# Performance work log

Measured on AMD Instinct MI355X. Metric: run time of the kernel, lower is better.

## Reference

```python
import jax, jax.numpy as jnp
import numpy as np
from functools import partial

CONF_THRESH = 0.5
NMS_THRESH = 0.5
B, N, NUM_CLASSES = 2, 10647, 80


def setup_inputs() -> dict:
    key = jax.random.key(0)
    # [batch, num_bboxes, x,y,w,h,p_obj + 80 class scores], uniform in [0,1)
    x = jax.random.uniform(key, (B, N, 5 + NUM_CLASSES), dtype=jnp.float32)
    return {"x": x}


def _center_to_corner(b):
    # b: [N,4] = (cx, cy, w, h) -> (x1, y1, x2, y2)
    cx, cy, w, h = b[:, 0], b[:, 1], b[:, 2], b[:, 3]
    return jnp.stack([cx - w / 2, cy - h / 2, cx + w / 2, cy + h / 2], axis=1)


def _pairwise_iou(b):
    # b: [N,4] corner boxes -> [N,N] IoU
    x1, y1, x2, y2 = b[:, 0], b[:, 1], b[:, 2], b[:, 3]
    ix1 = jnp.maximum(x1[:, None], x1[None, :])
    iy1 = jnp.maximum(y1[:, None], y1[None, :])
    ix2 = jnp.minimum(x2[:, None], x2[None, :])
    iy2 = jnp.minimum(y2[:, None], y2[None, :])
    inter = jnp.clip(ix2 - ix1, 0.0) * jnp.clip(iy2 - iy1, 0.0)
    area = (x2 - x1) * (y2 - y1)
    union = area[:, None] + area[None, :] - inter
    return inter / jnp.maximum(union, 1e-9)


def _nms_image(x_img, batch_idx):
    # x_img: [N, 5+C]. Faithful to the torch loop: conf-filter, per-class
    # greedy IoU suppression in descending-confidence order.
    n = x_img.shape[0]
    valid = x_img[:, 4] > CONF_THRESH
    xm = x_img * valid[:, None].astype(x_img.dtype)  # zero out background rows
    boxes = _center_to_corner(xm[:, :4])
    conf = xm[:, 4]
    score = jnp.max(xm[:, 5:], axis=1)
    cls = jnp.argmax(xm[:, 5:], axis=1)

    # Sort by confidence (descending) so greedy order matches the torch sort.
    order = jnp.argsort(-conf)
    boxes_s, cls_s, valid_s = boxes[order], cls[order], valid[order]

    # Suppression matrix: same class AND IoU >= threshold (constant wrt grads).
    iou = _pairwise_iou(boxes_s)                      # [N,N]
    same = cls_s[:, None] == cls_s[None, :]
    sup_mat = jax.lax.stop_gradient((iou >= NMS_THRESH) & same)

    idxs = jnp.arange(n)

    def body(i, keep):
        # box i (if still kept) suppresses lower-confidence same-class overlaps
        sup = keep[i] & (idxs > i) & sup_mat[i]
        return keep & ~sup

    keep_s = jax.lax.fori_loop(0, n, body, valid_s)
    keep = jnp.zeros(n, bool).at[order].set(keep_s)   # unsort

    km = keep[:, None].astype(x_img.dtype)
    bcol = jnp.full((n, 1), batch_idx, dtype=x_img.dtype) * km
    det = jnp.concatenate(
        [bcol, boxes * km, (conf * keep)[:, None],
         (score * keep)[:, None], (cls.astype(x_img.dtype) * keep)[:, None]],
        axis=1)  # [N, 8]: batch_idx, x1,y1,x2,y2, p_obj, max_conf, cls_idx
    return det


def reference(x) -> jnp.ndarray:
    batch_ids = jnp.arange(x.shape[0], dtype=x.dtype)
    # [B, N, 8]; suppressed / background rows are all-zero (fixed-shape analogue
    # of the variable-length torch detections tensor).
    return jax.vmap(_nms_image)(x, batch_ids)
```

## Files before the change

kernel.cpp:

```cpp
#include <hip/hip_runtime.h>
#include <stdint.h>

#define NROWS 10647
#define NFEAT 85
#define NCLS  80
#define NIMG  2
#define CONF_TH 0.5f
#define IOU_TH  0.5f
#define CAP    256
#define ROWS_PB 128

__global__ void k_zero(int* __restrict__ ccnt) {
    if (threadIdx.x < NIMG * NCLS) ccnt[threadIdx.x] = 0;
}

__global__ __launch_bounds__(256) void k_compact(
    const float* __restrict__ x, float4* __restrict__ bbox,
    float4* __restrict__ bmisc, int* __restrict__ ccnt, float* __restrict__ out) {
    __shared__ float buf[ROWS_PB * NFEAT];
    int img  = blockIdx.y;
    int base = blockIdx.x * ROWS_PB;
    int nrow = min(ROWS_PB, NROWS - base);
    int nflt = nrow * NFEAT;
    const float* g = x + ((size_t)img * NROWS + base) * NFEAT;
    const float4* g4 = (const float4*)g;
    float4* b4 = (float4*)buf;
    int nv = nflt >> 2;
    for (int i = threadIdx.x; i < nv; i += 256) b4[i] = g4[i];
    for (int i = (nv << 2) + threadIdx.x; i < nflt; i += 256) buf[i] = g[i];
    if (threadIdx.x < nrow) {
        float4 z = make_float4(0.f, 0.f, 0.f, 0.f);
        float4* o = (float4*)(out + ((size_t)img * NROWS + base + threadIdx.x) * 8);
        o[0] = z; o[1] = z;
    }
    __syncthreads();
    int t = threadIdx.x;
    if (t >= nrow) return;
    const float* row = buf + t * NFEAT;
    float conf = row[4];
    if (!(conf > CONF_TH)) return;
    float cx = row[0], cy = row[1], w = row[2], h = row[3];
    float4 b = make_float4(cx - w * 0.5f, cy - h * 0.5f,
                           cx + w * 0.5f, cy + h * 0.5f);
    float best = row[5];
    int cls = 0;
    for (int c = 1; c < NCLS; ++c) {
        float v = row[5 + c];
        if (v > best) { best = v; cls = c; }
    }
    int r = base + t;
    int pos = atomicAdd(&ccnt[img * NCLS + cls], 1);
    if (pos >= CAP) return;
    int idx = (img * NCLS + cls) * CAP + pos;
    bbox[idx]  = b;
    bmisc[idx] = make_float4(conf, best, (float)cls, __int_as_float(r));
}

__global__ __launch_bounds__(64) void k_nms(
    const float4* __restrict__ bbox, const float4* __restrict__ bmisc,
    const int* __restrict__ ccnt, float* __restrict__ out) {
    int cls = blockIdx.x, img = blockIdx.y;
    int mc = min(ccnt[img * NCLS + cls], CAP);
    if (mc == 0) return;
    int lane = threadIdx.x;
    int bse  = (img * NCLS + cls) * CAP;
    __shared__ uint64_t kl[CAP];
    __shared__ float4   sb[CAP];
    __shared__ float4   sm[CAP];

    float4 rb[4], rm[4];
    #pragma unroll
    for (int q = 0; q < 4; ++q) {
        int e = (q << 6) + lane;
        if (e < mc) {
            rb[q] = bbox[bse + e];
            rm[q] = bmisc[bse + e];
            uint32_t cbits = __float_as_uint(rm[q].x);
            kl[e] = ((uint64_t)(~cbits) << 32) | (uint32_t)__float_as_int(rm[q].w);
        }
    }
    __syncthreads();
    #pragma unroll
    for (int q = 0; q < 4; ++q) {
        int e = (q << 6) + lane;
        if (e < mc) {
            uint64_t k = kl[e];
            int rank = 0;
            for (int u = 0; u < mc; ++u) rank += (kl[u] < k);
            sb[rank] = rb[q];
            sm[rank] = rm[q];
        }
    }
    __syncthreads();
    float4 cb[4], cm[4];
    #pragma unroll
    for (int q = 0; q < 4; ++q) {
        int e = (q << 6) + lane;
        if (e < mc) { cb[q] = sb[e]; cm[q] = sm[e]; }
    }
    uint64_t km[4];
    #pragma unroll
    for (int q = 0; q < 4; ++q) {
        int lo = q << 6;
        km[q] = (mc >= lo + 64) ? ~0ull : (mc > lo ? ((1ull << (mc - lo)) - 1) : 0ull);
    }

#define SUPW(QI, QJ)                                                          \
    if ((QJ) * 64 < mc) {                                                     \
        bool s_ = false;                                                      \
        int j_ = ((QJ) << 6) + lane;                                          \
        if (j_ < mc && ((QJ) > (QI) || lane > li)) {                          \
            float bx = cb[QJ].x, by = cb[QJ].y, bz = cb[QJ].z, bw = cb[QJ].w; \
            float ix1 = fmaxf(ax, bx), iy1 = fmaxf(ay, by);                   \
            float ix2 = fminf(az, bz), iy2 = fminf(aw, bw);                   \
            float inter = fmaxf(ix2 - ix1, 0.f) * fmaxf(iy2 - iy1, 0.f);      \
            float ab = (bz - bx) * (bw - by);                                 \
            float iou = inter / fmaxf((aa + ab) - inter, 1e-9f);              \
            s_ = (iou >= IOU_TH);                                             \
        }                                                                     \
        km[QJ] &= ~__ballot(s_);                                              \
    }

#define RUNB(QI, SUPS)                                                        \
    if ((QI) * 64 < mc) {                                                     \
        int ilim = min(64, mc - ((QI) << 6));                                 \
        for (int li = 0; li < ilim; ++li) {                                   \
            if (!((km[QI] >> li) & 1ull)) continue;         \
            float ax = __shfl(cb[QI].x, li), ay = __shfl(cb[QI].y, li);       \
            float az = __shfl(cb[QI].z, li), aw = __shfl(cb[QI].w, li);       \
            float aa = (az - ax) * (aw - ay);                                 \
            SUPS                                                              \
        }                                                                     \
    }

    RUNB(0, SUPW(0,0) SUPW(0,1) SUPW(0,2) SUPW(0,3))
    RUNB(1, SUPW(1,1) SUPW(1,2) SUPW(1,3))
    RUNB(2, SUPW(2,2) SUPW(2,3))
    RUNB(3, SUPW(3,3))
#undef RUNB
#undef SUPW

    #pragma unroll
    for (int q = 0; q < 4; ++q) {
        int j = (q << 6) + lane;
        if (j < mc && ((km[q] >> lane) & 1ull)) {
            float4 b2 = cb[q];
            float4 mi = cm[q];
            int r = __float_as_int(mi.w);
            float* o = out + ((size_t)img * NROWS + r) * 8;
            o[0] = (float)img;
            o[1] = b2.x; o[2] = b2.y; o[3] = b2.z; o[4] = b2.w;
            o[5] = mi.x; o[6] = mi.y; o[7] = mi.z;
        }
    }
}

extern "C" void kernel_launch(void* const* d_in, const int* in_sizes, int n_in,
                              void* d_out, int out_size, void* d_ws, size_t ws_size,
                              hipStream_t stream) {
    const float* x = (const float*)d_in[0];
    float* out = (float*)d_out;

    char* w = (char*)d_ws;
    int*    ccnt  = (int*)w;
    float4* bbox  = (float4*)(w + 1024);
    float4* bmisc = (float4*)(w + 1024 + sizeof(float4) * NIMG * NCLS * CAP);

    k_zero<<<1, 256, 0, stream>>>(ccnt);

    dim3 g1((NROWS + ROWS_PB - 1) / ROWS_PB, NIMG);
    k_compact<<<g1, 256, 0, stream>>>(x, bbox, bmisc, ccnt, out);

    dim3 g2(NCLS, NIMG);
    k_nms<<<g2, 64, 0, stream>>>(bbox, bmisc, ccnt, out);
}
```

Measured before the change: 43.95 us.

## Drop zeroing kernel by resetting counters in NMS, shrink row blocks, split argmax

The separate counter-zeroing kernel launch is removed. Counters now live in global device memory and each NMS block resets its own counter after reading it. The compaction block size is halved to launch more blocks, output zeroing is spread across all threads, and the class argmax uses four independent chains to add instruction-level parallelism. The design relies on the counters being zero before the first call and on every nonzero counter being consumed each call.

```diff
diff --git a/kernel.cpp b/kernel.cpp
--- a/kernel.cpp
+++ b/kernel.cpp
@@ -8,15 +8,14 @@
 #define CONF_TH 0.5f
 #define IOU_TH  0.5f
 #define CAP    256
-#define ROWS_PB 128
+#define ROWS_PB 64
 
-__global__ void k_zero(int* __restrict__ ccnt) {
-    if (threadIdx.x < NIMG * NCLS) ccnt[threadIdx.x] = 0;
-}
+__device__ int    g_ccnt [NIMG * NCLS];
+__device__ float4 g_bbox [NIMG * NCLS * CAP];
+__device__ float4 g_bmisc[NIMG * NCLS * CAP];
 
 __global__ __launch_bounds__(256) void k_compact(
-    const float* __restrict__ x, float4* __restrict__ bbox,
-    float4* __restrict__ bmisc, int* __restrict__ ccnt, float* __restrict__ out) {
+    const float* __restrict__ x, float* __restrict__ out) {
     __shared__ float buf[ROWS_PB * NFEAT];
     int img  = blockIdx.y;
     int base = blockIdx.x * ROWS_PB;
@@ -28,10 +27,10 @@
     int nv = nflt >> 2;
     for (int i = threadIdx.x; i < nv; i += 256) b4[i] = g4[i];
     for (int i = (nv << 2) + threadIdx.x; i < nflt; i += 256) buf[i] = g[i];
-    if (threadIdx.x < nrow) {
+    {
         float4 z = make_float4(0.f, 0.f, 0.f, 0.f);
-        float4* o = (float4*)(out + ((size_t)img * NROWS + base + threadIdx.x) * 8);
-        o[0] = z; o[1] = z;
+        float4* o4 = (float4*)(out + ((size_t)img * NROWS + base) * 8);
+        for (int i = threadIdx.x; i < (nrow << 1); i += 256) o4[i] = z;
     }
     __syncthreads();
     int t = threadIdx.x;
@@ -42,28 +41,37 @@
     float cx = row[0], cy = row[1], w = row[2], h = row[3];
     float4 b = make_float4(cx - w * 0.5f, cy - h * 0.5f,
                            cx + w * 0.5f, cy + h * 0.5f);
-    float best = row[5];
-    int cls = 0;
-    for (int c = 1; c < NCLS; ++c) {
-        float v = row[5 + c];
-        if (v > best) { best = v; cls = c; }
+    float b0 = row[5], b1 = row[6], b2 = row[7], b3 = row[8];
+    int   i0 = 0, i1 = 1, i2 = 2, i3 = 3;
+    #pragma unroll
+    for (int c = 4; c < NCLS; c += 4) {
+        float v0 = row[5 + c], v1 = row[6 + c], v2 = row[7 + c], v3 = row[8 + c];
+        if (v0 > b0) { b0 = v0; i0 = c;     }
+        if (v1 > b1) { b1 = v1; i1 = c + 1; }
+        if (v2 > b2) { b2 = v2; i2 = c + 2; }
+        if (v3 > b3) { b3 = v3; i3 = c + 3; }
     }
+    float best = b0; int cls = i0;
+    if (b1 > best || (b1 == best && i1 < cls)) { best = b1; cls = i1; }
+    if (b2 > best || (b2 == best && i2 < cls)) { best = b2; cls = i2; }
+    if (b3 > best || (b3 == best && i3 < cls)) { best = b3; cls = i3; }
     int r = base + t;
-    int pos = atomicAdd(&ccnt[img * NCLS + cls], 1);
+    int pos = atomicAdd(&g_ccnt[img * NCLS + cls], 1);
     if (pos >= CAP) return;
     int idx = (img * NCLS + cls) * CAP + pos;
-    bbox[idx]  = b;
-    bmisc[idx] = make_float4(conf, best, (float)cls, __int_as_float(r));
+    g_bbox[idx]  = b;
+    g_bmisc[idx] = make_float4(conf, best, (float)cls, __int_as_float(r));
 }
 
-__global__ __launch_bounds__(64) void k_nms(
-    const float4* __restrict__ bbox, const float4* __restrict__ bmisc,
-    const int* __restrict__ ccnt, float* __restrict__ out) {
+__global__ __launch_bounds__(64) void k_nms(float* __restrict__ out) {
     int cls = blockIdx.x, img = blockIdx.y;
-    int mc = min(ccnt[img * NCLS + cls], CAP);
-    if (mc == 0) return;
+    int cidx = img * NCLS + cls;
+    int cnt  = g_ccnt[cidx];
+    if (cnt == 0) return;
+    if (threadIdx.x == 0) g_ccnt[cidx] = 0;
+    int mc = min(cnt, CAP);
     int lane = threadIdx.x;
-    int bse  = (img * NCLS + cls) * CAP;
+    int bse  = cidx * CAP;
     __shared__ uint64_t kl[CAP];
     __shared__ float4   sb[CAP];
     __shared__ float4   sm[CAP];
@@ -73,8 +81,8 @@
     for (int q = 0; q < 4; ++q) {
         int e = (q << 6) + lane;
         if (e < mc) {
-            rb[q] = bbox[bse + e];
-            rm[q] = bmisc[bse + e];
+            rb[q] = g_bbox[bse + e];
+            rm[q] = g_bmisc[bse + e];
             uint32_t cbits = __float_as_uint(rm[q].x);
             kl[e] = ((uint64_t)(~cbits) << 32) | (uint32_t)__float_as_int(rm[q].w);
         }
@@ -160,17 +168,11 @@
                               hipStream_t stream) {
     const float* x = (const float*)d_in[0];
     float* out = (float*)d_out;
-
-    char* w = (char*)d_ws;
-    int*    ccnt  = (int*)w;
-    float4* bbox  = (float4*)(w + 1024);
-    float4* bmisc = (float4*)(w + 1024 + sizeof(float4) * NIMG * NCLS * CAP);
-
-    k_zero<<<1, 256, 0, stream>>>(ccnt);
+    (void)d_ws; (void)ws_size;
 
     dim3 g1((NROWS + ROWS_PB - 1) / ROWS_PB, NIMG);
-    k_compact<<<g1, 256, 0, stream>>>(x, bbox, bmisc, ccnt, out);
+    k_compact<<<g1, 256, 0, stream>>>(x, out);
 
     dim3 g2(NCLS, NIMG);
-    k_nms<<<g2, 64, 0, stream>>>(bbox, bmisc, ccnt, out);
+    k_nms<<<g2, 64, 0, stream>>>(out);
 }
```

Result: faster. 39.49 us (-10.2%).
